# Optimization experiments

Measured on AMD Instinct MI355X. Metric: run time of the kernel, lower is better.

Reference implementation:

```python
import jax, jax.numpy as jnp
import numpy as np

N = 100000   # nodes (single node type 'A')
C = 256      # hidden_channels
OUT = 128    # out_channels
E_RAND = 300000  # random edges; total E = N + E_RAND = 400000
LN_EPS = 1e-5


def _linear_params(key, in_c, out_c):
    kw, kb = jax.random.split(key)
    bound = 1.0 / np.sqrt(in_c)
    W = jax.random.uniform(kw, (out_c, in_c), minval=-bound, maxval=bound, dtype=jnp.float32)
    b = jax.random.uniform(kb, (out_c,), minval=-bound, maxval=bound, dtype=jnp.float32)
    return W, b


def _edges(key):
    # guarantee every node appears in both rows -> unique()/remap in the torch
    # code is the identity, so the subgraph equals the full graph
    k0, k1 = jax.random.split(key)
    base = jnp.arange(N, dtype=jnp.int64)
    row0 = jnp.concatenate([base, jax.random.randint(k0, (E_RAND,), 0, N, dtype=jnp.int64)])
    row1 = jnp.concatenate([base, jax.random.randint(k1, (E_RAND,), 0, N, dtype=jnp.int64)])
    return jnp.stack([row0, row1])


def setup_inputs() -> dict:
    key = jax.random.key(0)
    ks = jax.random.split(key, 12)
    x = jax.random.normal(ks[0], (N, C), dtype=jnp.float32)
    edge_index_r0 = _edges(ks[1])
    edge_index_r1 = _edges(ks[2])
    wl0, bl0 = _linear_params(ks[3], C, C)
    w00, b00 = _linear_params(ks[4], C, C)
    w10, b10 = _linear_params(ks[5], C, C)
    wl1, bl1 = _linear_params(ks[6], C, C)
    w01, b01 = _linear_params(ks[7], C, C)
    w11, b11 = _linear_params(ks[8], C, C)
    Wout, bout = _linear_params(ks[9], C, OUT)
    return dict(
        x=x, edge_index_r0=edge_index_r0, edge_index_r1=edge_index_r1,
        wl0=wl0, bl0=bl0, w00=w00, b00=b00, w10=w10, b10=b10,
        gate0=jnp.float32(0.5), lns0=jnp.ones((C,), jnp.float32), lnb0=jnp.zeros((C,), jnp.float32),
        wl1=wl1, bl1=bl1, w01=w01, b01=b01, w11=w11, b11=b11,
        gate1=jnp.float32(0.5), lns1=jnp.ones((C,), jnp.float32), lnb1=jnp.zeros((C,), jnp.float32),
        Wout=Wout, bout=bout,
    )


def _metapath_layer(x0, h, ei, wl, bl, w0, b0, w1, b1, gate, lns, lnb):
    n = h.shape[0]
    src, dst = ei[0], ei[1]
    # PyG flow='target_to_source', aggr='add': message x_j = h[edge_index[1]],
    # scatter-added at edge_index[0]
    agg = jax.ops.segment_sum(h[dst], src, num_segments=n)
    # original code normalizes by bincount of edge_index[1] (kept faithfully)
    deg = jax.ops.segment_sum(jnp.ones_like(dst, dtype=h.dtype), dst, num_segments=n)
    agg = agg / jnp.clip(deg, 1.0)[:, None]
    g = jax.nn.sigmoid(gate)
    out = (agg @ wl.T + bl) + (1.0 - g) * (h @ w0.T + b0) + g * (x0 @ w1.T + b1)
    out = jax.nn.relu(out)
    mu = out.mean(-1, keepdims=True)
    var = out.var(-1, keepdims=True)
    out = (out - mu) / jnp.sqrt(var + LN_EPS) * lns + lnb
    return out  # dropout is identity in eval mode


def reference(x, edge_index_r0, edge_index_r1,
              wl0, bl0, w00, b00, w10, b10, gate0, lns0, lnb0,
              wl1, bl1, w01, b01, w11, b11, gate1, lns1, lnb1,
              Wout, bout):
    x0 = jax.lax.stop_gradient(x)  # x0_dict is detached in the torch code
    h = x
    # metapath is processed in reverse: conv index 1 first, then conv index 0
    h = _metapath_layer(x0, h, edge_index_r1, wl1, bl1, w01, b01, w11, b11, gate1, lns1, lnb1)
    h = _metapath_layer(x0, h, edge_index_r0, wl0, bl0, w00, b00, w10, b10, gate0, lns0, lnb0)
    return h @ Wout.T + bout
```

## Files before the change

### kernel.cpp

```cpp
#include <hip/hip_runtime.h>

typedef unsigned short u16;
typedef unsigned int   u32;

typedef __attribute__((ext_vector_type(8))) __bf16 bf16x8;
typedef __attribute__((ext_vector_type(8))) unsigned short u16x8;
typedef __attribute__((ext_vector_type(4))) float  f32x4;

#define C      256
#define OUTC   128
#define LN_EPS 1e-5f

__device__ __forceinline__ float bf2f(u16 u) {
    u32 i = ((u32)u) << 16; float f; __builtin_memcpy(&f, &i, 4); return f;
}
__device__ __forceinline__ u16 f2bf(float f) {
    u32 i; __builtin_memcpy(&i, &f, 4);
    u32 r = (i + 0x7FFFu + ((i >> 16) & 1u)) >> 16;
    return (u16)r;
}
__device__ __forceinline__ void load_lds16(const void* g, void* l) {
    __builtin_amdgcn_global_load_lds((const __attribute__((address_space(1))) u32*)g,
                                     (__attribute__((address_space(3))) u32*)l, 16, 0, 0);
}

#define PREP_BLK 1408
__global__ void prep_combo(const float* wl0, const float* w00, const float* w10,
                           const float* bl0, const float* b00, const float* b10,
                           const float* gate0,
                           const float* wl1, const float* w01, const float* w11,
                           const float* bl1, const float* b01, const float* b11,
                           const float* gate1,
                           const float* Wout, const float* x,
                           u16* __restrict__ WcatA, u16* __restrict__ WcatB,
                           u16* __restrict__ Woutb, float* __restrict__ bcat,
                           u16* __restrict__ xb, size_t n8)
{
    if (blockIdx.x >= PREP_BLK) {
        size_t i = ((size_t)(blockIdx.x - PREP_BLK) * 256 + threadIdx.x);
        if (i >= n8) return;
        const float* p = x + i * 8;
        float4 v0 = *(const float4*)p;
        float4 v1 = *(const float4*)(p + 4);
        u16x8 o;
        o[0] = f2bf(v0.x); o[1] = f2bf(v0.y); o[2] = f2bf(v0.z); o[3] = f2bf(v0.w);
        o[4] = f2bf(v1.x); o[5] = f2bf(v1.y); o[6] = f2bf(v1.z); o[7] = f2bf(v1.w);
        *(u16x8*)(xb + i * 8) = o;
        return;
    }
    int idx = blockIdx.x * 256 + threadIdx.x;
    float gA = 1.f / (1.f + expf(-gate1[0]));
    float gB = 1.f / (1.f + expf(-gate0[0]));
    if (idx < 256 * 512) {
        int n = idx >> 9, k = idx & 511;
        float v;
        if (k < 256) v = wl1[n * 256 + k];
        else         v = (1.f - gA) * w01[n * 256 + (k - 256)] + gA * w11[n * 256 + (k - 256)];
        WcatA[idx] = f2bf(v);
    } else if (idx < 256 * 512 + 256 * 768) {
        int j = idx - 256 * 512;
        int n = j / 768, k = j - n * 768;
        float v;
        if (k < 256)      v = wl0[n * 256 + k];
        else if (k < 512) v = (1.f - gB) * w00[n * 256 + (k - 256)];
        else              v = gB * w10[n * 256 + (k - 512)];
        WcatB[j] = f2bf(v);
    } else {
        int j = idx - (256 * 512 + 256 * 768);
        if (j < OUTC * C) Woutb[j] = f2bf(Wout[j]);
    }
    if (idx < 512) {
        int nn = idx & 255;
        if (idx < 256) bcat[idx] = bl1[nn] + (1.f - gA) * b01[nn] + gA * b11[nn];
        else           bcat[idx] = bl0[nn] + (1.f - gB) * b00[nn] + gB * b10[nn];
    }
}

__global__ void count_edges2(const int* __restrict__ ei1, const int* __restrict__ ei0,
                             int* __restrict__ cnt1, int* __restrict__ deg1,
                             int* __restrict__ cnt0, int* __restrict__ deg0,
                             int E, int Nn, int ebg)
{
    int b = blockIdx.x;
    const int* ei; int *cnt, *deg;
    if (b < ebg) { ei = ei1; cnt = cnt1; deg = deg1; }
    else         { b -= ebg; ei = ei0; cnt = cnt0; deg = deg0; }
    int idx = b * 256 + threadIdx.x;
    if (idx >= E) return;
    int s = ei[idx], d = ei[E + idx];
    if ((unsigned)s >= (unsigned)Nn || (unsigned)d >= (unsigned)Nn) return;
    atomicAdd(cnt + s, 1);
    atomicAdd(deg + d, 1);
}

__global__ void block_sums2(const int* __restrict__ cnt1, const int* __restrict__ cnt0,
                            int* __restrict__ parts1, int* __restrict__ parts0,
                            int n, int nblk)
{
    int b = blockIdx.x;
    const int* counts; int* partials;
    if (b < nblk) { counts = cnt1; partials = parts1; }
    else          { b -= nblk; counts = cnt0; partials = parts0; }
    int i = b * 256 + threadIdx.x;
    int v = (i < n) ? counts[i] : 0;
    #pragma unroll
    for (int off = 32; off; off >>= 1) v += __shfl_down(v, off, 64);
    __shared__ int ws[4];
    if ((threadIdx.x & 63) == 0) ws[threadIdx.x >> 6] = v;
    __syncthreads();
    if (threadIdx.x == 0) partials[b] = ws[0] + ws[1] + ws[2] + ws[3];
}

__global__ void scan_partials2(int* __restrict__ parts1, int* __restrict__ parts0, int nblk)
{
    int* partials = blockIdx.x ? parts0 : parts1;
    __shared__ int buf[1024];
    int tid = threadIdx.x;
    int v = (tid < nblk) ? partials[tid] : 0;
    buf[tid] = v; __syncthreads();
    for (int off = 1; off < 1024; off <<= 1) {
        int t = (tid >= off) ? buf[tid - off] : 0;
        __syncthreads();
        buf[tid] += t;
        __syncthreads();
    }
    if (tid < nblk) partials[tid] = buf[tid] - v;
}

__global__ void make_offsets2(int* __restrict__ cnt1, int* __restrict__ cnt0,
                              const int* __restrict__ parts1, const int* __restrict__ parts0,
                              int* __restrict__ off1a, int* __restrict__ off0a,
                              int n, int nblk)
{
    int b = blockIdx.x;
    int* counts_cursor; const int* partials; int* offsets;
    if (b < nblk) { counts_cursor = cnt1; partials = parts1; offsets = off1a; }
    else          { b -= nblk; counts_cursor = cnt0; partials = parts0; offsets = off0a; }
    __shared__ int buf[256];
    int i = b * 256 + threadIdx.x;
    int cnt = (i < n) ? counts_cursor[i] : 0;
    buf[threadIdx.x] = cnt; __syncthreads();
    for (int off = 1; off < 256; off <<= 1) {
        int t = (threadIdx.x >= off) ? buf[threadIdx.x - off] : 0;
        __syncthreads();
        buf[threadIdx.x] += t;
        __syncthreads();
    }
    int off = partials[b] + buf[threadIdx.x] - cnt;
    if (i < n) {
        offsets[i] = off;
        counts_cursor[i] = off;
        if (i == n - 1) offsets[n] = off + cnt;
    }
}

__global__ void fill_edges2(const int* __restrict__ ei1, const int* __restrict__ ei0,
                            int* __restrict__ cur1, int* __restrict__ cur0,
                            int* __restrict__ ed1, int* __restrict__ ed0,
                            int E, int Nn, int ebg)
{
    int b = blockIdx.x;
    const int* ei; int *cursor, *edgedst;
    if (b < ebg) { ei = ei1; cursor = cur1; edgedst = ed1; }
    else         { b -= ebg; ei = ei0; cursor = cur0; edgedst = ed0; }
    int idx = b * 256 + threadIdx.x;
    if (idx >= E) return;
    int s = ei[idx], d = ei[E + idx];
    if ((unsigned)s >= (unsigned)Nn || (unsigned)d >= (unsigned)Nn) return;
    int p = atomicAdd(cursor + s, 1);
    edgedst[p] = d;
}

__global__ __launch_bounds__(256) void gather_kernel(
    const int* __restrict__ offsets, const int* __restrict__ edgedst,
    const int* __restrict__ degcnt, const u16* __restrict__ h,
    u16* __restrict__ aggb, int Nn)
{
    int node = blockIdx.x * 4 + (threadIdx.x >> 6);
    if (node >= Nn) return;
    int lane = threadIdx.x & 63;
    int half = lane >> 5, l5 = lane & 31;
    int beg = offsets[node], end = offsets[node + 1];
    float a0[8] = {}, a1[8] = {};
    int p = beg;
    for (; p + 3 < end; p += 4) {
        int d0 = edgedst[p + half];
        int d1 = edgedst[p + 2 + half];
        u16x8 v0 = *(const u16x8*)(h + (size_t)d0 * C + l5 * 8);
        u16x8 v1 = *(const u16x8*)(h + (size_t)d1 * C + l5 * 8);
        #pragma unroll
        for (int j = 0; j < 8; ++j) { a0[j] += bf2f(v0[j]); a1[j] += bf2f(v1[j]); }
    }
    if (p + 1 < end) {
        int d0 = edgedst[p + half];
        u16x8 v0 = *(const u16x8*)(h + (size_t)d0 * C + l5 * 8);
        #pragma unroll
        for (int j = 0; j < 8; ++j) a0[j] += bf2f(v0[j]);
        p += 2;
    }
    if (p < end && half == 0) {
        int d0 = edgedst[p];
        u16x8 v0 = *(const u16x8*)(h + (size_t)d0 * C + l5 * 8);
        #pragma unroll
        for (int j = 0; j < 8; ++j) a1[j] += bf2f(v0[j]);
    }
    float inv = 1.0f / fmaxf((float)degcnt[node], 1.0f);
    u16x8 o;
    #pragma unroll
    for (int j = 0; j < 8; ++j) {
        float s = a0[j] + a1[j];
        s += __shfl_xor(s, 32);
        o[j] = f2bf(s * inv);
    }
    if (half == 0)
        *(u16x8*)(aggb + (size_t)node * C + l5 * 8) = o;
}

template <int NSEG, bool FUSE>
__global__ __launch_bounds__(512, 2) void layer_gemm8(
    const u16* __restrict__ s0, const u16* __restrict__ s1, const u16* __restrict__ s2,
    const u16* __restrict__ W,
    const float* __restrict__ bcat,
    const float* __restrict__ lns, const float* __restrict__ lnb,
    u16* __restrict__ Hout,
    const u16* __restrict__ WoutB, const float* __restrict__ boutp,
    float* __restrict__ outp, int Nnodes)
{
    constexpr int WK = NSEG * 256;
    constexpr int T  = NSEG * 4;

    extern __shared__ char smem[];
    u16*   A_e    = (u16*)smem;
    u16*   B_e    = (u16*)(smem + 65536);
    float* lnpart = (float*)(smem + 131072);
    u16*   h2l    = (u16*)smem;

    const int tid  = threadIdx.x;
    const int wave = tid >> 6, lane = tid & 63;
    const int wave_m = wave & 1, wave_n = wave >> 1;
    const int q = lane >> 4, l15 = lane & 15;
    const int m0 = blockIdx.x * 256;

    size_t a_goff[2], b_goff[2];
    int ldso[2];
    #pragma unroll
    for (int i = 0; i < 2; ++i) {
        int o = i * 8192 + wave * 1024 + lane * 16;
        int g = o >> 7, slot = (o >> 4) & 7;
        int bc = slot ^ (g & 7);
        int r = 2 * g + (bc >> 2), c = bc & 3;
        int node = m0 + r; if (node >= Nnodes) node = Nnodes - 1;
        a_goff[i] = (size_t)node * C + c * 8;
        b_goff[i] = (size_t)r * WK + c * 8;
        ldso[i]   = i * 8192 + wave * 1024;
    }

    int aoffE[8], boffE[4];
    #pragma unroll
    for (int j = 0; j < 8; ++j) {
        int r = wave_m * 128 + j * 16 + l15;
        aoffE[j] = (r >> 1) * 64 + (((((r & 1) << 2) | q) ^ ((r >> 1) & 7)) << 3);
    }
    #pragma unroll
    for (int f = 0; f < 4; ++f) {
        int r = wave_n * 64 + f * 16 + l15;
        boffE[f] = (r >> 1) * 64 + (((((r & 1) << 2) | q) ^ ((r >> 1) & 7)) << 3);
    }

    f32x4 acc[8][4] = {};

    auto stA = [&](int buf, int kh, int t) {
        const u16* sp = (t < 4) ? s0 : ((NSEG == 2 || t < 8) ? s1 : s2);
        const u16* base = sp + ((t & 3) << 6) + (kh << 5);
        #pragma unroll
        for (int i = 0; i < 2; ++i)
            load_lds16(base + a_goff[i], (char*)A_e + buf * 32768 + kh * 16384 + ldso[i]);
    };
    auto stB = [&](int buf, int kh, int t) {
        const u16* base = W + (t << 6) + (kh << 5);
        #pragma unroll
        for (int i = 0; i < 2; ++i)
            load_lds16(base + b_goff[i], (char*)B_e + buf * 32768 + kh * 16384 + ldso[i]);
    };

#define LDA(DST, BASE, MH) \
    _Pragma("unroll") for (int j = 0; j < 4; ++j) \
        DST[j] = *(const bf16x8*)((BASE) + aoffE[(MH) * 4 + j]);
#define LDB(DST, BASE) \
    _Pragma("unroll") for (int f = 0; f < 4; ++f) \
        DST[f] = *(const bf16x8*)((BASE) + boffE[f]);
#define MFMA16(MH, AF, BF) \
    _Pragma("unroll") for (int j = 0; j < 4; ++j) \
        _Pragma("unroll") for (int f = 0; f < 4; ++f) \
            acc[(MH) * 4 + j][f] = __builtin_amdgcn_mfma_f32_16x16x32_bf16( \
                AF[j], BF[f], acc[(MH) * 4 + j][f], 0, 0, 0);
#define SBAR()  asm volatile("s_barrier" ::: "memory")

    stA(0, 0, 0); stB(0, 0, 0); stA(0, 1, 0); stB(0, 1, 0);

    int cur = 0;
    for (int t = 0; t < T - 1; ++t, cur ^= 1) {
        const u16* Ac = A_e + cur * 16384;
        const u16* Bc = B_e + cur * 16384;
        const int nxt = cur ^ 1;
        bf16x8 af[4], bfr[4];
        stA(nxt, 0, t + 1); stB(nxt, 0, t + 1);
        asm volatile("s_waitcnt vmcnt(8)" ::: "memory");
        SBAR();
        __builtin_amdgcn_sched_barrier(0);
        LDB(bfr, Bc); LDA(af, Ac, 0);
        __builtin_amdgcn_s_setprio(1);
        MFMA16(0, af, bfr);
        __builtin_amdgcn_s_setprio(0);
        LDA(af, Ac, 1);
        __builtin_amdgcn_s_setprio(1);
        MFMA16(1, af, bfr);
        __builtin_amdgcn_s_setprio(0);
        SBAR();
        stA(nxt, 1, t + 1); stB(nxt, 1, t + 1);
        asm volatile("s_waitcnt vmcnt(8)" ::: "memory");
        SBAR();
        __builtin_amdgcn_sched_barrier(0);
        LDB(bfr, Bc + 8192); LDA(af, Ac + 8192, 0);
        __builtin_amdgcn_s_setprio(1);
        MFMA16(0, af, bfr);
        __builtin_amdgcn_s_setprio(0);
        LDA(af, Ac + 8192, 1);
        __builtin_amdgcn_s_setprio(1);
        MFMA16(1, af, bfr);
        __builtin_amdgcn_s_setprio(0);
        SBAR();
    }
    {
        const u16* Ac = A_e + cur * 16384;
        const u16* Bc = B_e + cur * 16384;
        bf16x8 af[4], bfr[4];
        asm volatile("s_waitcnt vmcnt(4)" ::: "memory");
        SBAR();
        __builtin_amdgcn_sched_barrier(0);
        LDB(bfr, Bc); LDA(af, Ac, 0);
        __builtin_amdgcn_s_setprio(1);
        MFMA16(0, af, bfr);
        __builtin_amdgcn_s_setprio(0);
        LDA(af, Ac, 1);
        __builtin_amdgcn_s_setprio(1);
        MFMA16(1, af, bfr);
        __builtin_amdgcn_s_setprio(0);
        SBAR();
        asm volatile("s_waitcnt vmcnt(0)" ::: "memory");
        SBAR();
        __builtin_amdgcn_sched_barrier(0);
        LDB(bfr, Bc + 8192); LDA(af, Ac + 8192, 0);
        __builtin_amdgcn_s_setprio(1);
        MFMA16(0, af, bfr);
        __builtin_amdgcn_s_setprio(0);
        LDA(af, Ac + 8192, 1);
        __builtin_amdgcn_s_setprio(1);
        MFMA16(1, af, bfr);
        __builtin_amdgcn_s_setprio(0);
    }

    float bias[4], lsc[4], lbi[4];
    #pragma unroll
    for (int f = 0; f < 4; ++f) {
        int n = wave_n * 64 + f * 16 + l15;
        bias[f] = bcat[n]; lsc[f] = lns[n]; lbi[f] = lnb[n];
    }
    #pragma unroll
    for (int t8 = 0; t8 < 8; ++t8)
        #pragma unroll
        for (int r = 0; r < 4; ++r) {
            float p = 0.f, pp = 0.f;
            #pragma unroll
            for (int f = 0; f < 4; ++f) {
                float v = acc[t8][f][r] + bias[f];
                v = fmaxf(v, 0.f);
                acc[t8][f][r] = v;
                p += v; pp += v * v;
            }
            #pragma unroll
            for (int off = 1; off < 16; off <<= 1) {
                p  += __shfl_xor(p,  off, 16);
                pp += __shfl_xor(pp, off, 16);
            }
            if (l15 == 0) {
                int row = wave_m * 128 + t8 * 16 + q * 4 + r;
                lnpart[row * 8 + wave_n * 2 + 0] = p;
                lnpart[row * 8 + wave_n * 2 + 1] = pp;
            }
        }
    __syncthreads();
    #pragma unroll
    for (int t8 = 0; t8 < 8; ++t8)
        #pragma unroll
        for (int r = 0; r < 4; ++r) {
            int row = wave_m * 128 + t8 * 16 + q * 4 + r;
            int node = m0 + row;
            float S1 = lnpart[row * 8 + 0] + lnpart[row * 8 + 2]
                     + lnpart[row * 8 + 4] + lnpart[row * 8 + 6];
            float S2 = lnpart[row * 8 + 1] + lnpart[row * 8 + 3]
                     + lnpart[row * 8 + 5] + lnpart[row * 8 + 7];
            float mean = S1 * (1.f / 256.f);
            float var  = fmaxf(S2 * (1.f / 256.f) - mean * mean, 0.f);
            float rstd = rsqrtf(var + LN_EPS);
            if constexpr (FUSE) {
                #pragma unroll
                for (int f = 0; f < 4; ++f) {
                    int n = wave_n * 64 + f * 16 + l15;
                    u16 hv = f2bf((acc[t8][f][r] - mean) * rstd * lsc[f] + lbi[f]);
                    h2l[row * 256 + (((n >> 3) ^ (row & 7)) << 3) + (n & 7)] = hv;
                }
            } else if (node < Nnodes) {
                u16* op = Hout + (size_t)node * C;
                #pragma unroll
                for (int f = 0; f < 4; ++f) {
                    int n = wave_n * 64 + f * 16 + l15;
                    op[n] = f2bf((acc[t8][f][r] - mean) * rstd * lsc[f] + lbi[f]);
                }
            }
        }

    if constexpr (FUSE) {
        __syncthreads();
        f32x4 acc2[8][2] = {};
        for (int kt = 0; kt < 8; ++kt) {
            bf16x8 bw[2];
            #pragma unroll
            for (int f = 0; f < 2; ++f) {
                int n = wave_n * 32 + f * 16 + l15;
                bw[f] = *(const bf16x8*)(WoutB + (size_t)n * 256 + kt * 32 + q * 8);
            }
            #pragma unroll
            for (int t8 = 0; t8 < 8; ++t8) {
                int row = wave_m * 128 + t8 * 16 + l15;
                bf16x8 a = *(const bf16x8*)(h2l + row * 256
                                            + ((((kt << 2) | q) ^ (row & 7)) << 3));
                #pragma unroll
                for (int f = 0; f < 2; ++f)
                    acc2[t8][f] = __builtin_amdgcn_mfma_f32_16x16x32_bf16(
                        a, bw[f], acc2[t8][f], 0, 0, 0);
            }
        }
        float b2[2];
        #pragma unroll
        for (int f = 0; f < 2; ++f) b2[f] = boutp[wave_n * 32 + f * 16 + l15];
        #pragma unroll
        for (int t8 = 0; t8 < 8; ++t8)
            #pragma unroll
            for (int r = 0; r < 4; ++r) {
                int row = wave_m * 128 + t8 * 16 + q * 4 + r;
                int node = m0 + row;
                if (node < Nnodes) {
                    float* op = outp + (size_t)node * OUTC;
                    #pragma unroll
                    for (int f = 0; f < 2; ++f)
                        op[wave_n * 32 + f * 16 + l15] = acc2[t8][f][r] + b2[f];
                }
            }
    }
#undef LDA
#undef LDB
#undef MFMA16
#undef SBAR
}

extern "C" void kernel_launch(void* const* d_in, const int* in_sizes, int n_in,
                              void* d_out, int out_size, void* d_ws, size_t ws_size,
                              hipStream_t stream)
{
    const float* x    = (const float*)d_in[0];
    const int*   ei0  = (const int*)d_in[1];
    const int*   ei1  = (const int*)d_in[2];
    const float* wl0  = (const float*)d_in[3];
    const float* bl0  = (const float*)d_in[4];
    const float* w00  = (const float*)d_in[5];
    const float* b00  = (const float*)d_in[6];
    const float* w10  = (const float*)d_in[7];
    const float* b10  = (const float*)d_in[8];
    const float* gate0= (const float*)d_in[9];
    const float* lns0 = (const float*)d_in[10];
    const float* lnb0 = (const float*)d_in[11];
    const float* wl1  = (const float*)d_in[12];
    const float* bl1  = (const float*)d_in[13];
    const float* w01  = (const float*)d_in[14];
    const float* b01  = (const float*)d_in[15];
    const float* w11  = (const float*)d_in[16];
    const float* b11  = (const float*)d_in[17];
    const float* gate1= (const float*)d_in[18];
    const float* lns1 = (const float*)d_in[19];
    const float* lnb1 = (const float*)d_in[20];
    const float* Wout = (const float*)d_in[21];
    const float* bout = (const float*)d_in[22];

    const int N = in_sizes[0] / C;
    const int E = in_sizes[1] / 2;

    char* w = (char*)d_ws;
    u16*   WcatA = (u16*)w;   w += (size_t)256 * 512 * 2;
    u16*   WcatB = (u16*)w;   w += (size_t)256 * 768 * 2;
    u16*   Woutb = (u16*)w;   w += (size_t)OUTC * C * 2;
    float* bcat  = (float*)w; w += 4096;
    int*   cnt1  = (int*)w;   w += (size_t)N * 4;
    int*   deg1  = (int*)w;   w += (size_t)N * 4;
    int*   cnt0  = (int*)w;   w += (size_t)N * 4;
    int*   deg0  = (int*)w;   w += (size_t)N * 4;
    int*   off1  = (int*)w;   w += (((size_t)(N + 1) * 4) + 255) & ~255ull;
    int*   off0  = (int*)w;   w += (((size_t)(N + 1) * 4) + 255) & ~255ull;
    int*   parts1= (int*)w;   w += 4096;
    int*   parts0= (int*)w;   w += 4096;
    int*   ed1   = (int*)w;   w += (size_t)E * 4;
    int*   ed0   = (int*)w;   w += (size_t)E * 4;
    u16*   xb    = (u16*)w;   w += (size_t)N * C * 2;
    u16*   aggb  = (u16*)w;   w += (size_t)N * C * 2;
    u16*   h1    = (u16*)w;   w += (size_t)N * C * 2;

    const int eb_grid = (E + 255) / 256;
    const int nblk    = (N + 255) / 256;
    const int gt_grid = (N + 3) / 4;
    const int gm8     = (N + 255) / 256;
    const size_t n8   = (size_t)N * C / 8;
    const int xc_blk  = (int)((n8 + 255) / 256);
    const size_t lds8 = 139264;

    hipMemsetAsync(cnt1, 0, (size_t)4 * N * 4, stream);
    prep_combo<<<PREP_BLK + xc_blk, 256, 0, stream>>>(
        wl0, w00, w10, bl0, b00, b10, gate0,
        wl1, w01, w11, bl1, b01, b11, gate1,
        Wout, x, WcatA, WcatB, Woutb, bcat, xb, n8);

    count_edges2 <<<2 * eb_grid, 256, 0, stream>>>(ei1, ei0, cnt1, deg1, cnt0, deg0, E, N, eb_grid);
    block_sums2  <<<2 * nblk, 256, 0, stream>>>(cnt1, cnt0, parts1, parts0, N, nblk);
    scan_partials2<<<2, 1024, 0, stream>>>(parts1, parts0, nblk);
    make_offsets2<<<2 * nblk, 256, 0, stream>>>(cnt1, cnt0, parts1, parts0, off1, off0, N, nblk);
    fill_edges2  <<<2 * eb_grid, 256, 0, stream>>>(ei1, ei0, cnt1, cnt0, ed1, ed0, E, N, eb_grid);

    gather_kernel<<<gt_grid, 256, 0, stream>>>(off1, ed1, deg1, xb, aggb, N);
    layer_gemm8<2, false><<<gm8, 512, lds8, stream>>>(aggb, xb, nullptr, WcatA, bcat,
                                                      lns1, lnb1, h1,
                                                      nullptr, nullptr, nullptr, N);

    gather_kernel<<<gt_grid, 256, 0, stream>>>(off0, ed0, deg0, h1, aggb, N);
    layer_gemm8<3, true><<<gm8, 512, lds8, stream>>>(aggb, h1, xb, WcatB, bcat + C,
                                                     lns0, lnb0, nullptr,
                                                     Woutb, bout, (float*)d_out, N);
}
```

Before: 528.6 us.

## Halve GEMM row tile, use 3-stage K pipeline, raise occupancy

The fused layer GEMM now works on 128-row tiles instead of 256, with a K step of 32 and a triple-buffered global-to-LDS pipeline gated by vmcnt waits. LDS use drops from about 136KB to 76KB and launch bounds move to 4 blocks per CU, aiming at more resident blocks and a grid of about 782 blocks rather than 391 to fill the CUs better. The fused output projection is split into two 64-row passes through a smaller LDS staging buffer. In exchange, each staged weight tile is reused across fewer rows, so weight traffic per node doubles, and the loop now runs twice as many barrier-synchronised iterations.

After: 619.6 us. 1.17x slower.

```diff
diff --git a/kernel.cpp b/kernel.cpp
--- a/kernel.cpp
+++ b/kernel.cpp
@@ -217,7 +217,7 @@
 }
 
 template <int NSEG, bool FUSE>
-__global__ __launch_bounds__(512, 2) void layer_gemm8(
+__global__ __launch_bounds__(512, 4) void layer_gemm9(
     const u16* __restrict__ s0, const u16* __restrict__ s1, const u16* __restrict__ s2,
     const u16* __restrict__ W,
     const float* __restrict__ bcat,
@@ -227,137 +227,86 @@
     float* __restrict__ outp, int Nnodes)
 {
     constexpr int WK = NSEG * 256;
-    constexpr int T  = NSEG * 4;
+    constexpr int T  = NSEG * 8;
 
     extern __shared__ char smem[];
     u16*   A_e    = (u16*)smem;
-    u16*   B_e    = (u16*)(smem + 65536);
-    float* lnpart = (float*)(smem + 131072);
-    u16*   h2l    = (u16*)smem;
+    u16*   B_e    = (u16*)(smem + 24576);
+    float* lnpart = (float*)(smem + 73728);
+    u16*   h2s    = (u16*)smem;
 
     const int tid  = threadIdx.x;
     const int wave = tid >> 6, lane = tid & 63;
     const int wave_m = wave & 1, wave_n = wave >> 1;
     const int q = lane >> 4, l15 = lane & 15;
-    const int m0 = blockIdx.x * 256;
-
-    size_t a_goff[2], b_goff[2];
-    int ldso[2];
+    const int m0 = blockIdx.x * 128;
+
+    size_t a_goff; int aldso;
+    {
+        int o = wave * 1024 + lane * 16;
+        int g = o >> 7, slot = (o >> 4) & 7;
+        int bc = slot ^ (g & 7);
+        int r = 2 * g + (bc >> 2), c = bc & 3;
+        int node = m0 + r; if (node >= Nnodes) node = Nnodes - 1;
+        a_goff = (size_t)node * C + c * 8;
+        aldso  = wave * 1024;
+    }
+    size_t b_goff[2]; int bldso[2];
     #pragma unroll
     for (int i = 0; i < 2; ++i) {
         int o = i * 8192 + wave * 1024 + lane * 16;
         int g = o >> 7, slot = (o >> 4) & 7;
         int bc = slot ^ (g & 7);
         int r = 2 * g + (bc >> 2), c = bc & 3;
-        int node = m0 + r; if (node >= Nnodes) node = Nnodes - 1;
-        a_goff[i] = (size_t)node * C + c * 8;
         b_goff[i] = (size_t)r * WK + c * 8;
-        ldso[i]   = i * 8192 + wave * 1024;
-    }
-
-    int aoffE[8], boffE[4];
-    #pragma unroll
-    for (int j = 0; j < 8; ++j) {
-        int r = wave_m * 128 + j * 16 + l15;
+        bldso[i]  = i * 8192 + wave * 1024;
+    }
+
+    int aoffE[4], boffE[4];
+    #pragma unroll
+    for (int j = 0; j < 4; ++j) {
+        int r = wave_m * 64 + j * 16 + l15;
         aoffE[j] = (r >> 1) * 64 + (((((r & 1) << 2) | q) ^ ((r >> 1) & 7)) << 3);
-    }
-    #pragma unroll
-    for (int f = 0; f < 4; ++f) {
-        int r = wave_n * 64 + f * 16 + l15;
-        boffE[f] = (r >> 1) * 64 + (((((r & 1) << 2) | q) ^ ((r >> 1) & 7)) << 3);
-    }
-
-    f32x4 acc[8][4] = {};
-
-    auto stA = [&](int buf, int kh, int t) {
-        const u16* sp = (t < 4) ? s0 : ((NSEG == 2 || t < 8) ? s1 : s2);
-        const u16* base = sp + ((t & 3) << 6) + (kh << 5);
-        #pragma unroll
-        for (int i = 0; i < 2; ++i)
-            load_lds16(base + a_goff[i], (char*)A_e + buf * 32768 + kh * 16384 + ldso[i]);
+        int rb = wave_n * 64 + j * 16 + l15;
+        boffE[j] = (rb >> 1) * 64 + (((((rb & 1) << 2) | q) ^ ((rb >> 1) & 7)) << 3);
+    }
+
+    f32x4 acc[4][4] = {};
+
+    auto stage = [&](int bi, int t) {
+        const u16* sp = (t < 8) ? s0 : ((NSEG == 2 || t < 16) ? s1 : s2);
+        load_lds16(sp + ((t & 7) << 5) + a_goff, (char*)A_e + bi * 8192 + aldso);
+        const u16* wb = W + (t << 5);
+        load_lds16(wb + b_goff[0], (char*)B_e + bi * 16384 + bldso[0]);
+        load_lds16(wb + b_goff[1], (char*)B_e + bi * 16384 + bldso[1]);
     };
-    auto stB = [&](int buf, int kh, int t) {
-        const u16* base = W + (t << 6) + (kh << 5);
-        #pragma unroll
-        for (int i = 0; i < 2; ++i)
-            load_lds16(base + b_goff[i], (char*)B_e + buf * 32768 + kh * 16384 + ldso[i]);
+    auto compute = [&](const u16* Ac, const u16* Bc) {
+        bf16x8 af[4], bfr[4];
+        #pragma unroll
+        for (int f = 0; f < 4; ++f) bfr[f] = *(const bf16x8*)(Bc + boffE[f]);
+        #pragma unroll
+        for (int j = 0; j < 4; ++j) af[j] = *(const bf16x8*)(Ac + aoffE[j]);
+        __builtin_amdgcn_s_setprio(1);
+        #pragma unroll
+        for (int j = 0; j < 4; ++j)
+            #pragma unroll
+            for (int f = 0; f < 4; ++f)
+                acc[j][f] = __builtin_amdgcn_mfma_f32_16x16x32_bf16(af[j], bfr[f], acc[j][f], 0, 0, 0);
+        __builtin_amdgcn_s_setprio(0);
     };
 
-#define LDA(DST, BASE, MH) \
-    _Pragma("unroll") for (int j = 0; j < 4; ++j) \
-        DST[j] = *(const bf16x8*)((BASE) + aoffE[(MH) * 4 + j]);
-#define LDB(DST, BASE) \
-    _Pragma("unroll") for (int f = 0; f < 4; ++f) \
-        DST[f] = *(const bf16x8*)((BASE) + boffE[f]);
-#define MFMA16(MH, AF, BF) \
-    _Pragma("unroll") for (int j = 0; j < 4; ++j) \
-        _Pragma("unroll") for (int f = 0; f < 4; ++f) \
-            acc[(MH) * 4 + j][f] = __builtin_amdgcn_mfma_f32_16x16x32_bf16( \
-                AF[j], BF[f], acc[(MH) * 4 + j][f], 0, 0, 0);
-#define SBAR()  asm volatile("s_barrier" ::: "memory")
-
-    stA(0, 0, 0); stB(0, 0, 0); stA(0, 1, 0); stB(0, 1, 0);
-
-    int cur = 0;
-    for (int t = 0; t < T - 1; ++t, cur ^= 1) {
-        const u16* Ac = A_e + cur * 16384;
-        const u16* Bc = B_e + cur * 16384;
-        const int nxt = cur ^ 1;
-        bf16x8 af[4], bfr[4];
-        stA(nxt, 0, t + 1); stB(nxt, 0, t + 1);
-        asm volatile("s_waitcnt vmcnt(8)" ::: "memory");
-        SBAR();
+    stage(0, 0); stage(1, 1); stage(2, 2);
+    int bi = 0;
+    for (int t = 0; t < T; ++t) {
+        if (t < T - 2)       asm volatile("s_waitcnt vmcnt(6)" ::: "memory");
+        else if (t == T - 2) asm volatile("s_waitcnt vmcnt(3)" ::: "memory");
+        else                 asm volatile("s_waitcnt vmcnt(0)" ::: "memory");
+        asm volatile("s_barrier" ::: "memory");
         __builtin_amdgcn_sched_barrier(0);
-        LDB(bfr, Bc); LDA(af, Ac, 0);
-        __builtin_amdgcn_s_setprio(1);
-        MFMA16(0, af, bfr);
-        __builtin_amdgcn_s_setprio(0);
-        LDA(af, Ac, 1);
-        __builtin_amdgcn_s_setprio(1);
-        MFMA16(1, af, bfr);
-        __builtin_amdgcn_s_setprio(0);
-        SBAR();
-        stA(nxt, 1, t + 1); stB(nxt, 1, t + 1);
-        asm volatile("s_waitcnt vmcnt(8)" ::: "memory");
-        SBAR();
-        __builtin_amdgcn_sched_barrier(0);
-        LDB(bfr, Bc + 8192); LDA(af, Ac + 8192, 0);
-        __builtin_amdgcn_s_setprio(1);
-        MFMA16(0, af, bfr);
-        __builtin_amdgcn_s_setprio(0);
-        LDA(af, Ac + 8192, 1);
-        __builtin_amdgcn_s_setprio(1);
-        MFMA16(1, af, bfr);
-        __builtin_amdgcn_s_setprio(0);
-        SBAR();
-    }
-    {
-        const u16* Ac = A_e + cur * 16384;
-        const u16* Bc = B_e + cur * 16384;
-        bf16x8 af[4], bfr[4];
-        asm volatile("s_waitcnt vmcnt(4)" ::: "memory");
-        SBAR();
-        __builtin_amdgcn_sched_barrier(0);
-        LDB(bfr, Bc); LDA(af, Ac, 0);
-        __builtin_amdgcn_s_setprio(1);
-        MFMA16(0, af, bfr);
-        __builtin_amdgcn_s_setprio(0);
-        LDA(af, Ac, 1);
-        __builtin_amdgcn_s_setprio(1);
-        MFMA16(1, af, bfr);
-        __builtin_amdgcn_s_setprio(0);
-        SBAR();
-        asm volatile("s_waitcnt vmcnt(0)" ::: "memory");
-        SBAR();
-        __builtin_amdgcn_sched_barrier(0);
-        LDB(bfr, Bc + 8192); LDA(af, Ac + 8192, 0);
-        __builtin_amdgcn_s_setprio(1);
-        MFMA16(0, af, bfr);
-        __builtin_amdgcn_s_setprio(0);
-        LDA(af, Ac + 8192, 1);
-        __builtin_amdgcn_s_setprio(1);
-        MFMA16(1, af, bfr);
-        __builtin_amdgcn_s_setprio(0);
+        compute(A_e + bi * 4096, B_e + bi * 8192);
+        asm volatile("s_barrier" ::: "memory");
+        if (t + 3 < T) stage(bi, t + 3);
+        bi = (bi == 2) ? 0 : bi + 1;
     }
 
     float bias[4], lsc[4], lbi[4];
@@ -367,15 +316,15 @@
         bias[f] = bcat[n]; lsc[f] = lns[n]; lbi[f] = lnb[n];
     }
     #pragma unroll
-    for (int t8 = 0; t8 < 8; ++t8)
+    for (int j = 0; j < 4; ++j)
         #pragma unroll
         for (int r = 0; r < 4; ++r) {
             float p = 0.f, pp = 0.f;
             #pragma unroll
             for (int f = 0; f < 4; ++f) {
-                float v = acc[t8][f][r] + bias[f];
+                float v = acc[j][f][r] + bias[f];
                 v = fmaxf(v, 0.f);
-                acc[t8][f][r] = v;
+                acc[j][f][r] = v;
                 p += v; pp += v * v;
             }
             #pragma unroll
@@ -384,17 +333,17 @@
                 pp += __shfl_xor(pp, off, 16);
             }
             if (l15 == 0) {
-                int row = wave_m * 128 + t8 * 16 + q * 4 + r;
+                int row = wave_m * 64 + j * 16 + q * 4 + r;
                 lnpart[row * 8 + wave_n * 2 + 0] = p;
                 lnpart[row * 8 + wave_n * 2 + 1] = pp;
             }
         }
     __syncthreads();
     #pragma unroll
-    for (int t8 = 0; t8 < 8; ++t8)
+    for (int j = 0; j < 4; ++j)
         #pragma unroll
         for (int r = 0; r < 4; ++r) {
-            int row = wave_m * 128 + t8 * 16 + q * 4 + r;
+            int row = wave_m * 64 + j * 16 + q * 4 + r;
             int node = m0 + row;
             float S1 = lnpart[row * 8 + 0] + lnpart[row * 8 + 2]
                      + lnpart[row * 8 + 4] + lnpart[row * 8 + 6];
@@ -405,63 +354,74 @@
             float rstd = rsqrtf(var + LN_EPS);
             if constexpr (FUSE) {
                 #pragma unroll
-                for (int f = 0; f < 4; ++f) {
-                    int n = wave_n * 64 + f * 16 + l15;
-                    u16 hv = f2bf((acc[t8][f][r] - mean) * rstd * lsc[f] + lbi[f]);
-                    h2l[row * 256 + (((n >> 3) ^ (row & 7)) << 3) + (n & 7)] = hv;
-                }
+                for (int f = 0; f < 4; ++f)
+                    acc[j][f][r] = (acc[j][f][r] - mean) * rstd * lsc[f] + lbi[f];
             } else if (node < Nnodes) {
                 u16* op = Hout + (size_t)node * C;
                 #pragma unroll
                 for (int f = 0; f < 4; ++f) {
                     int n = wave_n * 64 + f * 16 + l15;
-                    op[n] = f2bf((acc[t8][f][r] - mean) * rstd * lsc[f] + lbi[f]);
+                    op[n] = f2bf((acc[j][f][r] - mean) * rstd * lsc[f] + lbi[f]);
                 }
             }
         }
 
     if constexpr (FUSE) {
-        __syncthreads();
-        f32x4 acc2[8][2] = {};
-        for (int kt = 0; kt < 8; ++kt) {
-            bf16x8 bw[2];
-            #pragma unroll
-            for (int f = 0; f < 2; ++f) {
-                int n = wave_n * 32 + f * 16 + l15;
-                bw[f] = *(const bf16x8*)(WoutB + (size_t)n * 256 + kt * 32 + q * 8);
+        const int m2 = wave & 1, n2 = wave >> 1;
+        float b2[2];
+        #pragma unroll
+        for (int f2 = 0; f2 < 2; ++f2) b2[f2] = boutp[n2 * 32 + f2 * 16 + l15];
+        #pragma unroll
+        for (int s = 0; s < 2; ++s) {
+            __syncthreads();
+            if (wave_m == s) {
+                #pragma unroll
+                for (int j = 0; j < 4; ++j)
+                    #pragma unroll
+                    for (int r = 0; r < 4; ++r) {
+                        int rowl = j * 16 + q * 4 + r;
+                        #pragma unroll
+                        for (int f = 0; f < 4; ++f) {
+                            int n = wave_n * 64 + f * 16 + l15;
+                            h2s[rowl * 256 + ((((n >> 3) ^ (rowl & 15)) << 3) | (n & 7))]
+                                = f2bf(acc[j][f][r]);
+                        }
+                    }
+            }
+            __syncthreads();
+            f32x4 acc2[2][2] = {};
+            for (int kt = 0; kt < 8; ++kt) {
+                bf16x8 bw[2];
+                #pragma unroll
+                for (int f2 = 0; f2 < 2; ++f2)
+                    bw[f2] = *(const bf16x8*)(WoutB
+                              + (size_t)(n2 * 32 + f2 * 16 + l15) * 256 + kt * 32 + q * 8);
+                #pragma unroll
+                for (int mf2 = 0; mf2 < 2; ++mf2) {
+                    int rr = m2 * 32 + mf2 * 16 + l15;
+                    int ch = ((kt << 2) | q) ^ (rr & 15);
+                    bf16x8 a = *(const bf16x8*)(h2s + rr * 256 + (ch << 3));
+                    #pragma unroll
+                    for (int f2 = 0; f2 < 2; ++f2)
+                        acc2[mf2][f2] = __builtin_amdgcn_mfma_f32_16x16x32_bf16(
+                            a, bw[f2], acc2[mf2][f2], 0, 0, 0);
+                }
             }
             #pragma unroll
-            for (int t8 = 0; t8 < 8; ++t8) {
-                int row = wave_m * 128 + t8 * 16 + l15;
-                bf16x8 a = *(const bf16x8*)(h2l + row * 256
-                                            + ((((kt << 2) | q) ^ (row & 7)) << 3));
+            for (int mf2 = 0; mf2 < 2; ++mf2)
                 #pragma unroll
-                for (int f = 0; f < 2; ++f)
-                    acc2[t8][f] = __builtin_amdgcn_mfma_f32_16x16x32_bf16(
-                        a, bw[f], acc2[t8][f], 0, 0, 0);
-            }
+                for (int r = 0; r < 4; ++r) {
+                    int row = s * 64 + m2 * 32 + mf2 * 16 + q * 4 + r;
+                    int node = m0 + row;
+                    if (node < Nnodes) {
+                        float* op = outp + (size_t)node * OUTC;
+                        #pragma unroll
+                        for (int f2 = 0; f2 < 2; ++f2)
+                            op[n2 * 32 + f2 * 16 + l15] = acc2[mf2][f2][r] + b2[f2];
+                    }
+                }
         }
-        float b2[2];
-        #pragma unroll
-        for (int f = 0; f < 2; ++f) b2[f] = boutp[wave_n * 32 + f * 16 + l15];
-        #pragma unroll
-        for (int t8 = 0; t8 < 8; ++t8)
-            #pragma unroll
-            for (int r = 0; r < 4; ++r) {
-                int row = wave_m * 128 + t8 * 16 + q * 4 + r;
-                int node = m0 + row;
-                if (node < Nnodes) {
-                    float* op = outp + (size_t)node * OUTC;
-                    #pragma unroll
-                    for (int f = 0; f < 2; ++f)
-                        op[wave_n * 32 + f * 16 + l15] = acc2[t8][f][r] + b2[f];
-                }
-            }
-    }
-#undef LDA
-#undef LDB
-#undef MFMA16
-#undef SBAR
+    }
 }
 
 extern "C" void kernel_launch(void* const* d_in, const int* in_sizes, int n_in,
@@ -517,10 +477,10 @@
     const int eb_grid = (E + 255) / 256;
     const int nblk    = (N + 255) / 256;
     const int gt_grid = (N + 3) / 4;
-    const int gm8     = (N + 255) / 256;
+    const int gm9     = (N + 127) / 128;
     const size_t n8   = (size_t)N * C / 8;
     const int xc_blk  = (int)((n8 + 255) / 256);
-    const size_t lds8 = 139264;
+    const size_t lds9 = 77824;
 
     hipMemsetAsync(cnt1, 0, (size_t)4 * N * 4, stream);
     prep_combo<<<PREP_BLK + xc_blk, 256, 0, stream>>>(
@@ -535,12 +495,12 @@
     fill_edges2  <<<2 * eb_grid, 256, 0, stream>>>(ei1, ei0, cnt1, cnt0, ed1, ed0, E, N, eb_grid);
 
     gather_kernel<<<gt_grid, 256, 0, stream>>>(off1, ed1, deg1, xb, aggb, N);
-    layer_gemm8<2, false><<<gm8, 512, lds8, stream>>>(aggb, xb, nullptr, WcatA, bcat,
+    layer_gemm9<2, false><<<gm9, 512, lds9, stream>>>(aggb, xb, nullptr, WcatA, bcat,
                                                       lns1, lnb1, h1,
                                                       nullptr, nullptr, nullptr, N);
 
     gather_kernel<<<gt_grid, 256, 0, stream>>>(off0, ed0, deg0, h1, aggb, N);
-    layer_gemm8<3, true><<<gm8, 512, lds8, stream>>>(aggb, h1, xb, WcatB, bcat + C,
+    layer_gemm9<3, true><<<gm9, 512, lds9, stream>>>(aggb, h1, xb, WcatB, bcat + C,
                                                      lns0, lnb0, nullptr,
                                                      Woutb, bout, (float*)d_out, N);
 }
```
